# Kernel optimization log

Measured on AMD Instinct MI355X. Metric: run time of the kernel, lower is better.

## Reference

```python
import jax, jax.numpy as jnp
import numpy as np

B, C, H, W = 64, 256, 64, 64
HEADS = 8
Q = 16
FH = 512
EPS = 1e-6


def setup_inputs() -> dict:
    key = jax.random.key(0)
    ks = jax.random.split(key, 4)
    def init(k, shape, fan_in):
        return jax.random.normal(k, shape, jnp.float32) * (1.0 / np.sqrt(fan_in))
    return {
        "x": jax.random.normal(ks[0], (B, C, H, W), jnp.float32),
        "ln_gamma": jnp.ones((C,), jnp.float32),
        "ln_beta": jnp.zeros((C,), jnp.float32),
        # grouped 1x1 conv weight: torch shape [Q*h, C/h, 1, 1] -> [h, Q, C/h]
        "attn_w": init(ks[1], (HEADS, Q, C // HEADS), C // HEADS),
        "val_w": init(ks[2], (C, C), C),
        "val_b": jnp.zeros((C,), jnp.float32),
        "fin_w": init(ks[3], (FH, C * Q), C * Q),
        "fin_b": jnp.zeros((FH,), jnp.float32),
    }


def reference(x, ln_gamma, ln_beta, attn_w, val_w, val_b, fin_w, fin_b):
    B_, C_, H_, W_ = x.shape
    L = H_ * W_
    xf = x.reshape(B_, C_, L)  # [B, C, HW]
    # LayerNorm2d: normalize over channel dim (permute in torch == axis=1 here)
    mu = jnp.mean(xf, axis=1, keepdims=True)
    var = jnp.mean((xf - mu) ** 2, axis=1, keepdims=True)
    xn = (xf - mu) * jax.lax.rsqrt(var + EPS) * ln_gamma[:, None] + ln_beta[:, None]
    # grouped 1x1 conv: each head sees its own C/h channel slice
    xh = xn.reshape(B_, HEADS, C_ // HEADS, L)
    logits = jnp.einsum('hqc,bhcl->bhql', attn_w, xh)  # [B, h, Q, HW]
    Aw = jax.nn.softmax(logits, axis=-1)
    # value projection: full 1x1 conv with bias
    V = jnp.einsum('ec,bcl->bel', val_w, xn) + val_b[None, :, None]  # [B, C, HW]
    Vh = V.reshape(B_, HEADS, C_ // HEADS, L)
    # weighted pooling (bmm): [B, h, Q, d]
    A = jnp.einsum('bhql,bhdl->bhqd', Aw, Vh)
    Aflat = A.reshape(B_, Q * C_)  # matches torch reshape order (h, q, d)
    return Aflat @ fin_w.T + fin_b
```

## Files before the change

kernel.cpp:

```cpp
#include <hip/hip_runtime.h>

typedef unsigned short u16;
typedef unsigned int u32;

#define B_   64
#define C_   256
#define L_   4096
#define NH   8
#define NQ   16
#define DH   32
#define HQ   128
#define FHN  512
#define EPS_ 1e-6f

#define WS_WC    0
#define WS_SWG   8192
#define WS_CB    8704
#define WS_VGC   9216
#define WS_WG1   140288
#define WS_WB1   141312
#define WS_DENP  142336
#define WS_SNUP  404480
#define WS_A     666624
#define WS_APART 1715200

typedef __attribute__((ext_vector_type(8))) short bf16x8;
typedef __attribute__((ext_vector_type(4))) float f32x4;

__device__ __forceinline__ u16 f32_to_bf16(float f) {
    u32 u = __float_as_uint(f);
    u32 r = u + 0x7fffu + ((u >> 16) & 1u);
    return (u16)(r >> 16);
}
__device__ __forceinline__ float bf16_to_f32(u16 h) {
    return __uint_as_float(((u32)h) << 16);
}
__device__ __forceinline__ u32 pk2(u16 lo, u16 hi) {
    return (u32)lo | ((u32)hi << 16);
}

__global__ __launch_bounds__(256) void k_prep(
    const float* __restrict__ attn_w, const float* __restrict__ gamma,
    const float* __restrict__ beta, u16* __restrict__ wc,
    float* __restrict__ Swg, float* __restrict__ Cb)
{
    int t = threadIdx.x;
    if (t >= HQ) return;
    int h = t >> 4;
    float sw = 0.f, cb = 0.f;
    for (int c = 0; c < DH; c++) {
        float w = attn_w[t * DH + c];
        u16 hb = f32_to_bf16(w * gamma[h * DH + c]);
        wc[t * DH + c] = hb;
        sw += bf16_to_f32(hb);
        cb += w * beta[h * DH + c];
    }
    Swg[t] = sw;
    Cb[t] = cb;
}

__global__ __launch_bounds__(256) void k_prepv(
    const float* __restrict__ val_w, const float* __restrict__ gamma,
    const float* __restrict__ beta, u16* __restrict__ VGc,
    float* __restrict__ Wg1, float* __restrict__ Wb1)
{
    int t = threadIdx.x;
    int e = blockIdx.x * 4 + (t >> 6);
    int lane = t & 63;
    float4 w  = *(const float4*)(val_w + (size_t)e * C_ + lane * 4);
    float4 g  = *(const float4*)(gamma + lane * 4);
    float4 bt = *(const float4*)(beta + lane * 4);
    u16 h0 = f32_to_bf16(w.x * g.x);
    u16 h1 = f32_to_bf16(w.y * g.y);
    u16 h2 = f32_to_bf16(w.z * g.z);
    u16 h3 = f32_to_bf16(w.w * g.w);
    uint2 pk;
    pk.x = pk2(h0, h1);
    pk.y = pk2(h2, h3);
    *(uint2*)(VGc + (size_t)e * C_ + lane * 4) = pk;
    float sg = bf16_to_f32(h0) + bf16_to_f32(h1) + bf16_to_f32(h2) + bf16_to_f32(h3);
    float sb = w.x * bt.x + w.y * bt.y + w.z * bt.z + w.w * bt.w;
    #pragma unroll
    for (int off = 1; off < 64; off <<= 1) {
        sg += __shfl_xor(sg, off);
        sb += __shfl_xor(sb, off);
    }
    if (lane == 0) { Wg1[e] = sg; Wb1[e] = sb; }
}

__global__ __launch_bounds__(512, 2) void k_fused(
    const float* __restrict__ x, const u16* __restrict__ wc,
    const float* __restrict__ Swg, const float* __restrict__ Cb,
    const u16* __restrict__ VGc, float* __restrict__ Apart,
    float* __restrict__ DenP, float* __restrict__ SnuP)
{
    __shared__ __align__(16) char POOL[42496];
    u16* const XT = (u16*)POOL;
    u16* const EA = (u16*)(POOL + 16896);
    u16* const XC = (u16*)(POOL + 26112);
    __shared__ float smu[32], srs[32];
    int t = threadIdx.x;
    int lane = t & 63, wv = t >> 6;
    int lane15 = lane & 15, quad = lane >> 4;
    int ks = blockIdx.x, b = blockIdx.y;
    int lbase = ks * 512;
    int m0 = (wv & 1) * 64, n0 = (wv >> 1) * 64;
    int c_own = t & 255, hh = t >> 8;

    int h = wv;
    bf16x8 af = *(const bf16x8*)(wc + (size_t)(h * 16 + lane15) * DH + quad * 8);
    float swr[4], cbr[4];
    #pragma unroll
    for (int r = 0; r < 4; r++) {
        int hq = h * 16 + quad * 4 + r;
        swr[r] = Swg[hq];
        cbr[r] = Cb[hq];
    }

    const float* xR = x + ((size_t)b * C_ + c_own) * L_ + lbase + hh * 16;

    float4 fr[4];
    uint4 pr[2];
    auto loadregs = [&](int k) {
        #pragma unroll
        for (int i = 0; i < 4; i++) fr[i] = *(const float4*)(xR + k * 32 + i * 4);
    };
    auto cvtregs = [&]() {
        const float* pf = (const float*)fr;
        u16 hb[16];
        #pragma unroll
        for (int e = 0; e < 16; e++) hb[e] = f32_to_bf16(pf[e]);
        #pragma unroll
        for (int i = 0; i < 2; i++) {
            uint4 w;
            w.x = pk2(hb[i * 8 + 0], hb[i * 8 + 1]);
            w.y = pk2(hb[i * 8 + 2], hb[i * 8 + 3]);
            w.z = pk2(hb[i * 8 + 4], hb[i * 8 + 5]);
            w.w = pk2(hb[i * 8 + 6], hb[i * 8 + 7]);
            pr[i] = w;
        }
    };
    auto write_xc = [&]() {
        #pragma unroll
        for (int i = 0; i < 2; i++) {
            int g = hh * 2 + i;
            *(uint4*)&XC[c_own * 32 + ((g ^ ((c_own >> 1) & 3)) * 8)] = pr[i];
        }
    };
    auto write_xt = [&]() {
        const u16* ph = (const u16*)pr;
        #pragma unroll
        for (int e = 0; e < 16; e++) XT[(hh * 16 + e) * 264 + c_own] = ph[e];
    };

    f32x4 acc[4][4];
    #pragma unroll
    for (int i = 0; i < 4; i++)
        #pragma unroll
        for (int j = 0; j < 4; j++) {
            f32x4 z = {0.f, 0.f, 0.f, 0.f};
            acc[i][j] = z;
        }
    float se[4] = {}, sm[4] = {};

    int l_loc = t >> 4, g16 = t & 15;

    loadregs(0);
    cvtregs();
    write_xt();
    loadregs(1);
    __syncthreads();

    for (int k = 0; k < 16; k++) {
        write_xc();
        {
            const u16* row = XT + l_loc * 264 + g16 * 16;
            float s = 0.f, q = 0.f;
            #pragma unroll
            for (int j = 0; j < 2; j++) {
                uint4 v = *(const uint4*)(row + j * 8);
                u32 ww[4] = {v.x, v.y, v.z, v.w};
                #pragma unroll
                for (int e = 0; e < 4; e++) {
                    float f0 = __uint_as_float(ww[e] << 16);
                    float f1 = __uint_as_float(ww[e] & 0xffff0000u);
                    s += f0 + f1;
                    q += f0 * f0 + f1 * f1;
                }
            }
            #pragma unroll
            for (int off = 1; off < 16; off <<= 1) {
                s += __shfl_xor(s, off);
                q += __shfl_xor(q, off);
            }
            if (g16 == 0) {
                float mm = s * (1.f / C_);
                float vv = fmaxf(q * (1.f / C_) - mm * mm, 0.f) + EPS_;
                smu[l_loc] = mm;
                srs[l_loc] = rsqrtf(vv);
            }
        }
        __syncthreads();

        #pragma unroll
        for (int half = 0; half < 2; half++) {
            float m_l = smu[half * 16 + lane15];
            float r_l = srs[half * 16 + lane15];
            bf16x8 bfrag = *(const bf16x8*)(XT + (half * 16 + lane15) * 264 + h * DH + quad * 8);
            f32x4 z = {0.f, 0.f, 0.f, 0.f};
            f32x4 c4 = __builtin_amdgcn_mfma_f32_16x16x32_bf16(af, bfrag, z, 0, 0, 0);
            #pragma unroll
            for (int r = 0; r < 4; r++) {
                float logit = r_l * (c4[r] - m_l * swr[r]) + cbr[r];
                float e = __expf(logit);
                float ers = e * r_l;
                EA[(h * 16 + quad * 4 + r) * 36 + half * 16 + lane15] = f32_to_bf16(ers);
                se[r] += e;
                sm[r] += ers * m_l;
            }
        }
        if (k < 15) cvtregs();
        if (k < 14) loadregs(k + 2);
        __syncthreads();

        bf16x8 a[4];
        #pragma unroll
        for (int i = 0; i < 4; i++)
            a[i] = *(const bf16x8*)&EA[(m0 + i * 16 + lane15) * 36 + quad * 8];
        #pragma unroll
        for (int j = 0; j < 4; j++) {
            int row = n0 + j * 16 + lane15;
            bf16x8 bbj = *(const bf16x8*)&XC[row * 32 + ((quad ^ ((row >> 1) & 3)) * 8)];
            #pragma unroll
            for (int i = 0; i < 4; i++)
                acc[i][j] = __builtin_amdgcn_mfma_f32_16x16x32_bf16(a[i], bbj, acc[i][j], 0, 0, 0);
        }
        if (k < 15) write_xt();
        __syncthreads();
    }

    u16* const P = (u16*)POOL;
    float* ApB = Apart + (((size_t)ks * B_ + b) * HQ) * DH;
    #pragma unroll
    for (int half = 0; half < 2; half++) {
        if ((wv & 1) == half) {
            #pragma unroll
            for (int i = 0; i < 4; i++)
                #pragma unroll
                for (int j = 0; j < 4; j++) {
                    int lr = i * 16 + quad * 4;
                    int col = n0 + j * 16 + lane15;
                    #pragma unroll
                    for (int r = 0; r < 4; r++)
                        P[(lr + r) * 264 + col] = f32_to_bf16(acc[i][j][r]);
                }
        }
        __syncthreads();
        {
            int hl = wv >> 1;
            int he = half * 4 + hl;
            int dt = wv & 1;
            f32x4 c2 = {0.f, 0.f, 0.f, 0.f};
            #pragma unroll
            for (int kk = 0; kk < 8; kk++) {
                bf16x8 a = *(const bf16x8*)&P[(hl * 16 + lane15) * 264 + kk * 32 + quad * 8];
                bf16x8 vg = *(const bf16x8*)(VGc + (size_t)(he * DH + dt * 16 + lane15) * C_ + kk * 32 + quad * 8);
                c2 = __builtin_amdgcn_mfma_f32_16x16x32_bf16(a, vg, c2, 0, 0, 0);
            }
            #pragma unroll
            for (int r = 0; r < 4; r++)
                ApB[(size_t)(he * 16 + quad * 4 + r) * DH + dt * 16 + lane15] = c2[r];
        }
        __syncthreads();
    }

    #pragma unroll
    for (int r = 0; r < 4; r++) {
        float v = se[r], w = sm[r];
        #pragma unroll
        for (int off = 1; off < 16; off <<= 1) {
            v += __shfl_xor(v, off);
            w += __shfl_xor(w, off);
        }
        if (lane15 == 0) {
            int row = b * HQ + wv * 16 + quad * 4 + r;
            DenP[ks * (B_ * HQ) + row] = v;
            SnuP[ks * (B_ * HQ) + row] = w;
        }
    }
}

__global__ __launch_bounds__(256) void k_reduce(
    const float* __restrict__ Apart, const float* __restrict__ DenP,
    const float* __restrict__ SnuP, const float* __restrict__ Wg1,
    const float* __restrict__ Wb1, const float* __restrict__ val_b,
    float* __restrict__ A)
{
    __shared__ float sden[32], ssnu[32];
    int t = threadIdx.x;
    int q4 = blockIdx.x, b = blockIdx.y;
    int hq0 = q4 * 32;
    if (t < 32) {
        int row = b * HQ + hq0 + t;
        float d = 0.f, sn = 0.f;
        #pragma unroll
        for (int s = 0; s < 8; s++) {
            d  += DenP[s * (B_ * HQ) + row];
            sn += SnuP[s * (B_ * HQ) + row];
        }
        sden[t] = d;
        ssnu[t] = sn;
    }
    __syncthreads();
    #pragma unroll
    for (int i = 0; i < 4; i++) {
        int idx = i * 256 + t;
        int r32 = idx >> 5, d = idx & 31;
        int hq = hq0 + r32;
        float v = 0.f;
        #pragma unroll
        for (int s = 0; s < 8; s++)
            v += Apart[(((size_t)s * B_ + b) * HQ + hq) * DH + d];
        int hd = (hq >> 4) * DH + d;
        A[((size_t)b * HQ + hq) * DH + d] =
            (v - ssnu[r32] * Wg1[hd]) / sden[r32] + Wb1[hd] + val_b[hd];
    }
}

__global__ __launch_bounds__(256) void k_final(
    const float* __restrict__ A, const float* __restrict__ fin_w,
    const float* __restrict__ fin_b, float* __restrict__ out)
{
    __shared__ float At[64 * 129];
    __shared__ float Fw[32 * 129];
    int t = threadIdx.x;
    int kc = blockIdx.x, ft = blockIdx.y;
    int k0 = kc * 128;

    #pragma unroll
    for (int w = 0; w < 8; w++) {
        int s = t + w * 256;
        int row = s >> 5, seg = s & 31;
        float4 v = *(const float4*)(A + (size_t)row * 4096 + k0 + seg * 4);
        const float* pf = (const float*)&v;
        #pragma unroll
        for (int e = 0; e < 4; e++) At[row * 129 + seg * 4 + e] = pf[e];
    }
    #pragma unroll
    for (int w = 0; w < 4; w++) {
        int s = t + w * 256;
        int row = s >> 5, seg = s & 31;
        float4 v = *(const float4*)(fin_w + (size_t)(ft * 32 + row) * 4096 + k0 + seg * 4);
        const float* pf = (const float*)&v;
        #pragma unroll
        for (int e = 0; e < 4; e++) Fw[row * 129 + seg * 4 + e] = pf[e];
    }
    __syncthreads();

    int tb = t >> 3, tf = t & 7;
    float acc[2][4];
    #pragma unroll
    for (int e = 0; e < 2; e++)
        #pragma unroll
        for (int j = 0; j < 4; j++) acc[e][j] = 0.f;

    for (int k = 0; k < 128; k++) {
        float a0 = At[(tb * 2) * 129 + k];
        float a1 = At[(tb * 2 + 1) * 129 + k];
        #pragma unroll
        for (int j = 0; j < 4; j++) {
            float f = Fw[(tf * 4 + j) * 129 + k];
            acc[0][j] += a0 * f;
            acc[1][j] += a1 * f;
        }
    }
    #pragma unroll
    for (int e = 0; e < 2; e++) {
        int brow = tb * 2 + e;
        #pragma unroll
        for (int j = 0; j < 4; j++) {
            int f = ft * 32 + tf * 4 + j;
            float v = acc[e][j];
            if (kc == 0) v += fin_b[f];
            atomicAdd(&out[(size_t)brow * FHN + f], v);
        }
    }
}

extern "C" void kernel_launch(void* const* d_in, const int* in_sizes, int n_in,
                              void* d_out, int out_size, void* d_ws, size_t ws_size,
                              hipStream_t stream) {
    const float* x      = (const float*)d_in[0];
    const float* gamma  = (const float*)d_in[1];
    const float* beta   = (const float*)d_in[2];
    const float* attn_w = (const float*)d_in[3];
    const float* val_w  = (const float*)d_in[4];
    const float* val_b  = (const float*)d_in[5];
    const float* fin_w  = (const float*)d_in[6];
    const float* fin_b  = (const float*)d_in[7];
    float* out = (float*)d_out;
    char* ws = (char*)d_ws;

    u16*   wc    = (u16*)(ws + WS_WC);
    float* Swg   = (float*)(ws + WS_SWG);
    float* Cb    = (float*)(ws + WS_CB);
    u16*   VGc   = (u16*)(ws + WS_VGC);
    float* Wg1   = (float*)(ws + WS_WG1);
    float* Wb1   = (float*)(ws + WS_WB1);
    float* DenP  = (float*)(ws + WS_DENP);
    float* SnuP  = (float*)(ws + WS_SNUP);
    float* A     = (float*)(ws + WS_A);
    float* Apart = (float*)(ws + WS_APART);

    hipMemsetAsync(out, 0, (size_t)B_ * FHN * sizeof(float), stream);

    k_prep<<<dim3(1), dim3(256), 0, stream>>>(attn_w, gamma, beta, wc, Swg, Cb);
    k_prepv<<<dim3(64), dim3(256), 0, stream>>>(val_w, gamma, beta, VGc, Wg1, Wb1);
    k_fused<<<dim3(8, 64), dim3(512), 0, stream>>>(x, wc, Swg, Cb, VGc, Apart,
                                                   DenP, SnuP);
    k_reduce<<<dim3(4, 64), dim3(256), 0, stream>>>(Apart, DenP, SnuP, Wg1, Wb1,
                                                    val_b, A);
    k_final<<<dim3(32, 16), dim3(256), 0, stream>>>(A, fin_w, fin_b, out);
}
```

Baseline: 441.2 us.

## Use 1024-thread blocks over 4 L-splits to halve split-K partials

The fused kernel now uses 1024-thread blocks, each covering 1024 spatial positions (4 splits instead of 8). Every iteration processes 64 positions as two 32-wide chunks, and the warps are re-tiled so each owns a 32x64 accumulator tile. Denominator and numerator sums from the two warp halves are combined in shared memory. The intent is to halve the partial outputs and the per-block epilogue (the value-projection MFMA and the Apart writes), at the cost of one block per CU with a larger LDS footprint. With only 256 blocks, per-CU occupancy and latency hiding may suffer.

```diff
diff --git a/kernel.cpp b/kernel.cpp
--- a/kernel.cpp
+++ b/kernel.cpp
@@ -11,6 +11,7 @@
 #define DH   32
 #define HQ   128
 #define FHN  512
+#define NKS  4
 #define EPS_ 1e-6f
 
 #define WS_WC    0
@@ -20,9 +21,9 @@
 #define WS_WG1   140288
 #define WS_WB1   141312
 #define WS_DENP  142336
-#define WS_SNUP  404480
-#define WS_A     666624
-#define WS_APART 1715200
+#define WS_SNUP  273408
+#define WS_A     404480
+#define WS_APART 1453056
 
 typedef __attribute__((ext_vector_type(8))) short bf16x8;
 typedef __attribute__((ext_vector_type(4))) float f32x4;
@@ -88,26 +89,25 @@
     if (lane == 0) { Wg1[e] = sg; Wb1[e] = sb; }
 }
 
-__global__ __launch_bounds__(512, 2) void k_fused(
+__global__ __launch_bounds__(1024, 1) void k_fused(
     const float* __restrict__ x, const u16* __restrict__ wc,
     const float* __restrict__ Swg, const float* __restrict__ Cb,
     const u16* __restrict__ VGc, float* __restrict__ Apart,
     float* __restrict__ DenP, float* __restrict__ SnuP)
 {
-    __shared__ __align__(16) char POOL[42496];
+    __shared__ __align__(16) char POOL[84992];
     u16* const XT = (u16*)POOL;
-    u16* const EA = (u16*)(POOL + 16896);
-    u16* const XC = (u16*)(POOL + 26112);
-    __shared__ float smu[32], srs[32];
+    u16* const EA = (u16*)(POOL + 33792);
+    u16* const XC = (u16*)(POOL + 52224);
+    __shared__ float smu[64], srs[64];
+    __shared__ float sred[256];
     int t = threadIdx.x;
-    int lane = t & 63, wv = t >> 6;
+    int lane = t & 63, w = t >> 6;
     int lane15 = lane & 15, quad = lane >> 4;
     int ks = blockIdx.x, b = blockIdx.y;
-    int lbase = ks * 512;
-    int m0 = (wv & 1) * 64, n0 = (wv >> 1) * 64;
-    int c_own = t & 255, hh = t >> 8;
-
-    int h = wv;
+    int c_own = t & 255, seg = t >> 8;
+
+    int h = w & 7, lw = w >> 3;
     bf16x8 af = *(const bf16x8*)(wc + (size_t)(h * 16 + lane15) * DH + quad * 8);
     float swr[4], cbr[4];
     #pragma unroll
@@ -117,13 +117,15 @@
         cbr[r] = Cb[hq];
     }
 
-    const float* xR = x + ((size_t)b * C_ + c_own) * L_ + lbase + hh * 16;
+    int m0 = (w & 3) * 32, n0 = (w >> 2) * 64;
+
+    const float* xR = x + ((size_t)b * C_ + c_own) * L_ + ks * 1024 + seg * 16;
 
     float4 fr[4];
     uint4 pr[2];
-    auto loadregs = [&](int k) {
-        #pragma unroll
-        for (int i = 0; i < 4; i++) fr[i] = *(const float4*)(xR + k * 32 + i * 4);
+    auto loadregs = [&](int g) {
+        #pragma unroll
+        for (int i = 0; i < 4; i++) fr[i] = *(const float4*)(xR + g * 64 + i * 4);
     };
     auto cvtregs = [&]() {
         const float* pf = (const float*)fr;
@@ -132,30 +134,31 @@
         for (int e = 0; e < 16; e++) hb[e] = f32_to_bf16(pf[e]);
         #pragma unroll
         for (int i = 0; i < 2; i++) {
-            uint4 w;
-            w.x = pk2(hb[i * 8 + 0], hb[i * 8 + 1]);
-            w.y = pk2(hb[i * 8 + 2], hb[i * 8 + 3]);
-            w.z = pk2(hb[i * 8 + 4], hb[i * 8 + 5]);
-            w.w = pk2(hb[i * 8 + 6], hb[i * 8 + 7]);
-            pr[i] = w;
+            uint4 wd;
+            wd.x = pk2(hb[i * 8 + 0], hb[i * 8 + 1]);
+            wd.y = pk2(hb[i * 8 + 2], hb[i * 8 + 3]);
+            wd.z = pk2(hb[i * 8 + 4], hb[i * 8 + 5]);
+            wd.w = pk2(hb[i * 8 + 6], hb[i * 8 + 7]);
+            pr[i] = wd;
         }
     };
     auto write_xc = [&]() {
+        int cn = seg >> 1, hh = seg & 1;
         #pragma unroll
         for (int i = 0; i < 2; i++) {
-            int g = hh * 2 + i;
-            *(uint4*)&XC[c_own * 32 + ((g ^ ((c_own >> 1) & 3)) * 8)] = pr[i];
+            int g8 = hh * 2 + i;
+            *(uint4*)&XC[cn * 8192 + c_own * 32 + ((g8 ^ ((c_own >> 1) & 3)) * 8)] = pr[i];
         }
     };
     auto write_xt = [&]() {
         const u16* ph = (const u16*)pr;
         #pragma unroll
-        for (int e = 0; e < 16; e++) XT[(hh * 16 + e) * 264 + c_own] = ph[e];
+        for (int e = 0; e < 16; e++) XT[(seg * 16 + e) * 264 + c_own] = ph[e];
     };
 
-    f32x4 acc[4][4];
-    #pragma unroll
-    for (int i = 0; i < 4; i++)
+    f32x4 acc[2][4];
+    #pragma unroll
+    for (int i = 0; i < 2; i++)
         #pragma unroll
         for (int j = 0; j < 4; j++) {
             f32x4 z = {0.f, 0.f, 0.f, 0.f};
@@ -171,7 +174,7 @@
     loadregs(1);
     __syncthreads();
 
-    for (int k = 0; k < 16; k++) {
+    for (int g = 0; g < 16; g++) {
         write_xc();
         {
             const u16* row = XT + l_loc * 264 + g16 * 16;
@@ -204,9 +207,10 @@
 
         #pragma unroll
         for (int half = 0; half < 2; half++) {
-            float m_l = smu[half * 16 + lane15];
-            float r_l = srs[half * 16 + lane15];
-            bf16x8 bfrag = *(const bf16x8*)(XT + (half * 16 + lane15) * 264 + h * DH + quad * 8);
+            int row = lw * 32 + half * 16 + lane15;
+            float m_l = smu[row];
+            float r_l = srs[row];
+            bf16x8 bfrag = *(const bf16x8*)(XT + row * 264 + h * DH + quad * 8);
             f32x4 z = {0.f, 0.f, 0.f, 0.f};
             f32x4 c4 = __builtin_amdgcn_mfma_f32_16x16x32_bf16(af, bfrag, z, 0, 0, 0);
             #pragma unroll
@@ -214,79 +218,83 @@
                 float logit = r_l * (c4[r] - m_l * swr[r]) + cbr[r];
                 float e = __expf(logit);
                 float ers = e * r_l;
-                EA[(h * 16 + quad * 4 + r) * 36 + half * 16 + lane15] = f32_to_bf16(ers);
+                EA[(h * 16 + quad * 4 + r) * 72 + lw * 36 + half * 16 + lane15] = f32_to_bf16(ers);
                 se[r] += e;
                 sm[r] += ers * m_l;
             }
         }
-        if (k < 15) cvtregs();
-        if (k < 14) loadregs(k + 2);
+        if (g < 15) cvtregs();
+        if (g < 14) loadregs(g + 2);
         __syncthreads();
 
-        bf16x8 a[4];
-        #pragma unroll
-        for (int i = 0; i < 4; i++)
-            a[i] = *(const bf16x8*)&EA[(m0 + i * 16 + lane15) * 36 + quad * 8];
+        #pragma unroll
+        for (int cn = 0; cn < 2; cn++) {
+            bf16x8 a0 = *(const bf16x8*)&EA[(m0 + lane15) * 72 + cn * 36 + quad * 8];
+            bf16x8 a1 = *(const bf16x8*)&EA[(m0 + 16 + lane15) * 72 + cn * 36 + quad * 8];
+            #pragma unroll
+            for (int j = 0; j < 4; j++) {
+                int row = n0 + j * 16 + lane15;
+                bf16x8 bbj = *(const bf16x8*)&XC[cn * 8192 + row * 32 + ((quad ^ ((row >> 1) & 3)) * 8)];
+                acc[0][j] = __builtin_amdgcn_mfma_f32_16x16x32_bf16(a0, bbj, acc[0][j], 0, 0, 0);
+                acc[1][j] = __builtin_amdgcn_mfma_f32_16x16x32_bf16(a1, bbj, acc[1][j], 0, 0, 0);
+            }
+        }
+        if (g < 15) write_xt();
+        __syncthreads();
+    }
+
+    #pragma unroll
+    for (int r = 0; r < 4; r++) {
+        #pragma unroll
+        for (int off = 1; off < 16; off <<= 1) {
+            se[r] += __shfl_xor(se[r], off);
+            sm[r] += __shfl_xor(sm[r], off);
+        }
+    }
+    int hqr = h * 16 + quad * 4;
+    if (lane15 == 0 && lw == 1) {
+        #pragma unroll
+        for (int r = 0; r < 4; r++) {
+            sred[hqr + r] = se[r];
+            sred[128 + hqr + r] = sm[r];
+        }
+    }
+    __syncthreads();
+    if (lane15 == 0 && lw == 0) {
+        #pragma unroll
+        for (int r = 0; r < 4; r++) {
+            int row = b * HQ + hqr + r;
+            DenP[ks * (B_ * HQ) + row] = se[r] + sred[hqr + r];
+            SnuP[ks * (B_ * HQ) + row] = sm[r] + sred[128 + hqr + r];
+        }
+    }
+    __syncthreads();
+
+    u16* const P = (u16*)POOL;
+    #pragma unroll
+    for (int i = 0; i < 2; i++)
         #pragma unroll
         for (int j = 0; j < 4; j++) {
-            int row = n0 + j * 16 + lane15;
-            bf16x8 bbj = *(const bf16x8*)&XC[row * 32 + ((quad ^ ((row >> 1) & 3)) * 8)];
-            #pragma unroll
-            for (int i = 0; i < 4; i++)
-                acc[i][j] = __builtin_amdgcn_mfma_f32_16x16x32_bf16(a[i], bbj, acc[i][j], 0, 0, 0);
-        }
-        if (k < 15) write_xt();
-        __syncthreads();
-    }
-
-    u16* const P = (u16*)POOL;
-    float* ApB = Apart + (((size_t)ks * B_ + b) * HQ) * DH;
-    #pragma unroll
-    for (int half = 0; half < 2; half++) {
-        if ((wv & 1) == half) {
-            #pragma unroll
-            for (int i = 0; i < 4; i++)
-                #pragma unroll
-                for (int j = 0; j < 4; j++) {
-                    int lr = i * 16 + quad * 4;
-                    int col = n0 + j * 16 + lane15;
-                    #pragma unroll
-                    for (int r = 0; r < 4; r++)
-                        P[(lr + r) * 264 + col] = f32_to_bf16(acc[i][j][r]);
-                }
-        }
-        __syncthreads();
-        {
-            int hl = wv >> 1;
-            int he = half * 4 + hl;
-            int dt = wv & 1;
-            f32x4 c2 = {0.f, 0.f, 0.f, 0.f};
-            #pragma unroll
-            for (int kk = 0; kk < 8; kk++) {
-                bf16x8 a = *(const bf16x8*)&P[(hl * 16 + lane15) * 264 + kk * 32 + quad * 8];
-                bf16x8 vg = *(const bf16x8*)(VGc + (size_t)(he * DH + dt * 16 + lane15) * C_ + kk * 32 + quad * 8);
-                c2 = __builtin_amdgcn_mfma_f32_16x16x32_bf16(a, vg, c2, 0, 0, 0);
-            }
+            int prow = m0 + i * 16 + quad * 4;
+            int col = n0 + j * 16 + lane15;
             #pragma unroll
             for (int r = 0; r < 4; r++)
-                ApB[(size_t)(he * 16 + quad * 4 + r) * DH + dt * 16 + lane15] = c2[r];
-        }
-        __syncthreads();
-    }
-
-    #pragma unroll
-    for (int r = 0; r < 4; r++) {
-        float v = se[r], w = sm[r];
-        #pragma unroll
-        for (int off = 1; off < 16; off <<= 1) {
-            v += __shfl_xor(v, off);
-            w += __shfl_xor(w, off);
-        }
-        if (lane15 == 0) {
-            int row = b * HQ + wv * 16 + quad * 4 + r;
-            DenP[ks * (B_ * HQ) + row] = v;
-            SnuP[ks * (B_ * HQ) + row] = w;
-        }
+                P[(prow + r) * 264 + col] = f32_to_bf16(acc[i][j][r]);
+        }
+    __syncthreads();
+    {
+        int he = w >> 1, dt = w & 1;
+        f32x4 c2 = {0.f, 0.f, 0.f, 0.f};
+        #pragma unroll
+        for (int kk = 0; kk < 8; kk++) {
+            bf16x8 a = *(const bf16x8*)&P[(he * 16 + lane15) * 264 + kk * 32 + quad * 8];
+            bf16x8 vg = *(const bf16x8*)(VGc + (size_t)(he * DH + dt * 16 + lane15) * C_ + kk * 32 + quad * 8);
+            c2 = __builtin_amdgcn_mfma_f32_16x16x32_bf16(a, vg, c2, 0, 0, 0);
+        }
+        float* ApB = Apart + (((size_t)ks * B_ + b) * HQ) * DH;
+        #pragma unroll
+        for (int r = 0; r < 4; r++)
+            ApB[(size_t)(he * 16 + quad * 4 + r) * DH + dt * 16 + lane15] = c2[r];
     }
 }
 
@@ -304,7 +312,7 @@
         int row = b * HQ + hq0 + t;
         float d = 0.f, sn = 0.f;
         #pragma unroll
-        for (int s = 0; s < 8; s++) {
+        for (int s = 0; s < NKS; s++) {
             d  += DenP[s * (B_ * HQ) + row];
             sn += SnuP[s * (B_ * HQ) + row];
         }
@@ -319,7 +327,7 @@
         int hq = hq0 + r32;
         float v = 0.f;
         #pragma unroll
-        for (int s = 0; s < 8; s++)
+        for (int s = 0; s < NKS; s++)
             v += Apart[(((size_t)s * B_ + b) * HQ + hq) * DH + d];
         int hd = (hq >> 4) * DH + d;
         A[((size_t)b * HQ + hq) * DH + d] =
@@ -416,8 +424,8 @@
 
     k_prep<<<dim3(1), dim3(256), 0, stream>>>(attn_w, gamma, beta, wc, Swg, Cb);
     k_prepv<<<dim3(64), dim3(256), 0, stream>>>(val_w, gamma, beta, VGc, Wg1, Wb1);
-    k_fused<<<dim3(8, 64), dim3(512), 0, stream>>>(x, wc, Swg, Cb, VGc, Apart,
-                                                   DenP, SnuP);
+    k_fused<<<dim3(NKS, 64), dim3(1024), 0, stream>>>(x, wc, Swg, Cb, VGc, Apart,
+                                                      DenP, SnuP);
     k_reduce<<<dim3(4, 64), dim3(256), 0, stream>>>(Apart, DenP, SnuP, Wg1, Wb1,
                                                     val_b, A);
     k_final<<<dim3(32, 16), dim3(256), 0, stream>>>(A, fin_w, fin_b, out);
```

Result: slower. 457.7 us (+3.7%).
